# Kernel tuning notes

Hardware: AMD Instinct MI355X
Metric: run time of the kernel (lower is better)

## Reference

```python
import jax, jax.numpy as jnp
import numpy as np

B, A, F, C = 32, 64, 128, 128


def _mlp(h, W0, b0, W1, b1):
    # LinearLayer stack: Linear(2F->C) + ReLU, Linear(C->C) + ReLU
    h = jax.nn.relu(h @ W0 + b0)
    h = jax.nn.relu(h @ W1 + b1)
    return h


def setup_inputs() -> dict:
    key = jax.random.key(0)
    k0, k1, k2 = jax.random.split(key, 3)
    x = jax.random.normal(k0, (B, A, F), dtype=jnp.float32)
    W0 = jax.random.normal(k1, (2 * F, C), dtype=jnp.float32) * (1.0 / np.sqrt(2 * F))
    b0 = jnp.zeros((C,), dtype=jnp.float32)
    W1 = jax.random.normal(k2, (C, C), dtype=jnp.float32) * (1.0 / np.sqrt(C))
    b1 = jnp.zeros((C,), dtype=jnp.float32)
    return {"x": x, "W0": W0, "b0": b0, "W1": W1, "b1": b1}


def reference(x, W0, b0, W1, b1):
    nb, na, nf = x.shape
    # atom_tile[b,i,j]   = x[b,i]  (first atom of the pair)
    # atom_repeat[b,i,j] = x[b,j]  (second atom of the pair)
    xi = jnp.broadcast_to(x[:, :, None, :], (nb, na, na, nf))
    xj = jnp.broadcast_to(x[:, None, :, :], (nb, na, na, nf))
    # pair_x0 = cat(atom_tile, atom_repeat) = [x_i, x_j]
    p0 = jnp.concatenate([xi, xj], axis=-1).reshape(nb * na * na, 2 * nf)
    # pair_x1 = cat(atom_repeat, atom_tile) = [x_j, x_i]
    p1 = jnp.concatenate([xj, xi], axis=-1).reshape(nb * na * na, 2 * nf)
    h0 = _mlp(p0, W0, b0, W1, b1).reshape(nb, na * na, -1)
    h1 = _mlp(p1, W0, b0, W1, b1).reshape(nb, na * na, -1)
    return h0 + h1
```

## Files before the change

### kernel.cpp

```cpp
#include <hip/hip_runtime.h>
#include <hip/hip_bf16.h>

typedef float    f32x4 __attribute__((ext_vector_type(4)));
typedef _Float16 f16x8 __attribute__((ext_vector_type(8)));
typedef unsigned int   u32x4 __attribute__((ext_vector_type(4)));
typedef unsigned short u16x4 __attribute__((ext_vector_type(4)));

#define NB 32
#define NA 64
#define NF 128
#define NC 128

__global__ __launch_bounds__(512) void prep_kernel(
    const float* __restrict__ x, const float* __restrict__ W0,
    const float* __restrict__ b0, const float* __restrict__ W1,
    _Float16* __restrict__ u, _Float16* __restrict__ v,
    _Float16* __restrict__ w1f)
{
    int blk = blockIdx.x;
    int tid = threadIdx.x;
    if (blk < 256) {
        __shared__ __align__(16) float xs[8 * 128];
        int b = blk >> 3;
        int g = blk & 7;
        if (tid < 256)
            ((f32x4*)xs)[tid] =
                ((const f32x4*)(x + (size_t)(b * NA + g * 8) * NF))[tid];
        __syncthreads();
        int c = tid & 127;
        int h = (tid >> 7) & 1;
        int s = tid >> 8;
        const float* wp = W0 + (size_t)h * 128 * NC + c;
        const float* xp = xs + s * 4 * 128;
        float a0 = 0.f, a1 = 0.f, a2 = 0.f, a3 = 0.f;
        #pragma unroll 8
        for (int f = 0; f < 128; ++f) {
            float w = wp[(size_t)f * NC];
            a0 = fmaf(xp[f],       w, a0);
            a1 = fmaf(xp[128 + f], w, a1);
            a2 = fmaf(xp[256 + f], w, a2);
            a3 = fmaf(xp[384 + f], w, a3);
        }
        int row = b * NA + g * 8 + s * 4;
        if (h == 0) {
            u[(size_t)(row + 0) * NC + c] = (_Float16)a0;
            u[(size_t)(row + 1) * NC + c] = (_Float16)a1;
            u[(size_t)(row + 2) * NC + c] = (_Float16)a2;
            u[(size_t)(row + 3) * NC + c] = (_Float16)a3;
        } else {
            float bb = b0[c];
            v[(size_t)(row + 0) * NC + c] = (_Float16)(a0 + bb);
            v[(size_t)(row + 1) * NC + c] = (_Float16)(a1 + bb);
            v[(size_t)(row + 2) * NC + c] = (_Float16)(a2 + bb);
            v[(size_t)(row + 3) * NC + c] = (_Float16)(a3 + bb);
        }
    } else {
        int idx  = ((blk - 256) * 512 + tid) * 4;
        int e0   = idx & 7;
        int fl   = idx >> 3;
        int lane = fl & 63;
        int frag = fl >> 6;
        int kk = frag >> 3, nf = frag & 7;
        int k = kk * 32 + (lane >> 4) * 8 + e0;
        int n = nf * 16 + (lane & 15);
        u16x4 o;
        #pragma unroll
        for (int e = 0; e < 4; ++e) {
            _Float16 w = (_Float16)W1[(size_t)(k + e) * NC + n];
            o[e] = __builtin_bit_cast(unsigned short, w);
        }
        *(u16x4*)(w1f + idx) = o;
    }
}

__global__ __launch_bounds__(256, 3) void pair_mlp_kernel(
    const float* __restrict__ b1g, const _Float16* __restrict__ u,
    const _Float16* __restrict__ v, const _Float16* __restrict__ w1f,
    float* __restrict__ out)
{
    __shared__ __align__(16) _Float16 u_s[16 * 128];
    __shared__ __align__(16) _Float16 v_s[16 * 128];
    __shared__ __align__(16) _Float16 w_s[32 * 64 * 8];

    int blk = blockIdx.x;
    int b = blk / 36;
    int t = blk % 36;
    int I = 0;
    while (t >= 8 - I) { t -= 8 - I; ++I; }
    int J = I + t;

    int tid = threadIdx.x;

    {
        int row = tid >> 4;
        int c   = tid & 15;
        int ga  = b * NA + ((row < 8) ? (I * 8 + row) : (J * 8 + (row & 7)));
        ((u32x4*)u_s)[tid] = ((const u32x4*)(u + (size_t)ga * NC))[c];
        ((u32x4*)v_s)[tid] = ((const u32x4*)(v + (size_t)ga * NC))[c];
    }
    #pragma unroll
    for (int p = 0; p < 8; ++p)
        ((u32x4*)w_s)[p * 256 + tid] = ((const u32x4*)w1f)[p * 256 + tid];
    __syncthreads();

    int wave = tid >> 6;
    int lane = tid & 63;
    int llo  = lane & 15;
    int lhi  = lane >> 4;
    int r    = wave * 16 + llo;
    int il   = r >> 3;
    int jl   = r & 7;

    f32x4 acc0[8], acc1[8];
    f32x4 z = {0.f, 0.f, 0.f, 0.f};
    #pragma unroll
    for (int nf = 0; nf < 8; ++nf) { acc0[nf] = z; acc1[nf] = z; }

    const f16x8* uI = (const f16x8*)(u_s + il * 128);
    const f16x8* vI = (const f16x8*)(v_s + il * 128);
    const f16x8* uJ = (const f16x8*)(u_s + (8 + jl) * 128);
    const f16x8* vJ = (const f16x8*)(v_s + (8 + jl) * 128);
    const f16x8* wf = (const f16x8*)w_s;

    #pragma unroll
    for (int kk = 0; kk < 4; ++kk) {
        int kc = kk * 4 + lhi;

        f16x8 uIv = uI[kc];
        f16x8 vIv = vI[kc];
        f16x8 uJv = uJ[kc];
        f16x8 vJv = vJ[kc];

        f16x8 s0 = uIv + vJv;
        f16x8 s1 = uJv + vIv;
        f16x8 h0, h1;
        #pragma unroll
        for (int e = 0; e < 8; ++e) {
            h0[e] = s0[e] < (_Float16)0 ? (_Float16)0 : s0[e];
            h1[e] = s1[e] < (_Float16)0 ? (_Float16)0 : s1[e];
        }

        #pragma unroll
        for (int nf = 0; nf < 8; ++nf) {
            f16x8 w = wf[(kk * 8 + nf) * 64 + lane];
            acc0[nf] = __builtin_amdgcn_mfma_f32_16x16x32_f16(w, h0, acc0[nf], 0, 0, 0);
            acc1[nf] = __builtin_amdgcn_mfma_f32_16x16x32_f16(w, h1, acc1[nf], 0, 0, 0);
        }
    }

    int Ig = I * 8 + il;
    int Jg = J * 8 + jl;
    float* p1 = out + ((size_t)b * 4096 + Ig * 64 + Jg) * 128 + lhi * 4;
    float* p2 = out + ((size_t)b * 4096 + Jg * 64 + Ig) * 128 + lhi * 4;
    bool mirror = (I != J);
    #pragma unroll
    for (int nf = 0; nf < 8; ++nf) {
        f32x4 bias = *(const f32x4*)(b1g + nf * 16 + lhi * 4);
        f32x4 val;
        #pragma unroll
        for (int e = 0; e < 4; ++e)
            val[e] = fmaxf(acc0[nf][e] + bias[e], 0.f) +
                     fmaxf(acc1[nf][e] + bias[e], 0.f);
        *(f32x4*)(p1 + nf * 16) = val;
        if (mirror)
            *(f32x4*)(p2 + nf * 16) = val;
    }
}

extern "C" void kernel_launch(void* const* d_in, const int* in_sizes, int n_in,
                              void* d_out, int out_size, void* d_ws, size_t ws_size,
                              hipStream_t stream)
{
    (void)in_sizes; (void)n_in; (void)out_size; (void)ws_size;
    const float* x  = (const float*)d_in[0];
    const float* W0 = (const float*)d_in[1];
    const float* b0 = (const float*)d_in[2];
    const float* W1 = (const float*)d_in[3];
    const float* b1 = (const float*)d_in[4];
    float* out = (float*)d_out;

    _Float16* u   = (_Float16*)d_ws;
    _Float16* v   = u + (size_t)NB * NA * NC;
    _Float16* w1f = v + (size_t)NB * NA * NC;

    prep_kernel<<<264, 512, 0, stream>>>(x, W0, b0, W1, u, v, w1f);
    pair_mlp_kernel<<<32 * 36, 256, 0, stream>>>(b1, u, v, w1f, out);
}
```

Baseline: 32.33 us.

## Use MFMA for W0 projection in prep kernel and swizzle pair-kernel LDS

```diff
diff --git a/kernel.cpp b/kernel.cpp
--- a/kernel.cpp
+++ b/kernel.cpp
@@ -2,74 +2,104 @@
 #include <hip/hip_bf16.h>
 
 typedef float    f32x4 __attribute__((ext_vector_type(4)));
+typedef _Float16 f16x4 __attribute__((ext_vector_type(4)));
 typedef _Float16 f16x8 __attribute__((ext_vector_type(8)));
 typedef unsigned int   u32x4 __attribute__((ext_vector_type(4)));
-typedef unsigned short u16x4 __attribute__((ext_vector_type(4)));
 
 #define NB 32
 #define NA 64
 #define NF 128
 #define NC 128
 
-__global__ __launch_bounds__(512) void prep_kernel(
+__global__ __launch_bounds__(256) void prep_kernel(
     const float* __restrict__ x, const float* __restrict__ W0,
     const float* __restrict__ b0, const float* __restrict__ W1,
     _Float16* __restrict__ u, _Float16* __restrict__ v,
     _Float16* __restrict__ w1f)
 {
-    int blk = blockIdx.x;
-    int tid = threadIdx.x;
+    int blk = blockIdx.x, tid = threadIdx.x;
     if (blk < 256) {
-        __shared__ __align__(16) float xs[8 * 128];
-        int b = blk >> 3;
-        int g = blk & 7;
-        if (tid < 256)
-            ((f32x4*)xs)[tid] =
-                ((const f32x4*)(x + (size_t)(b * NA + g * 8) * NF))[tid];
+        __shared__ __align__(16) _Float16 w0h[32 * 64 * 8];
+        int b = blk >> 3, g = (blk >> 1) & 3, half = blk & 1;
+
+        int lane = tid & 63, wave = tid >> 6;
+        int llo = lane & 15, lhi = lane >> 4;
+
+        const float* xrow = x + ((size_t)b * NA + g * 16 + llo) * NF;
+        f16x8 xf[4];
+        #pragma unroll
+        for (int kk = 0; kk < 4; ++kk) {
+            f32x4 a0 = *(const f32x4*)(xrow + kk * 32 + lhi * 8);
+            f32x4 a1 = *(const f32x4*)(xrow + kk * 32 + lhi * 8 + 4);
+            #pragma unroll
+            for (int e = 0; e < 4; ++e) {
+                xf[kk][e]     = (_Float16)a0[e];
+                xf[kk][e + 4] = (_Float16)a1[e];
+            }
+        }
+
+        #pragma unroll
+        for (int p = 0; p < 8; ++p) {
+            int sl   = p * 256 + tid;
+            int frag = sl >> 6;
+            int ln   = sl & 63;
+            int kk   = frag >> 3, nfc = frag & 7;
+            int k0   = half * 128 + kk * 32 + (ln >> 4) * 8;
+            int c    = nfc * 16 + (ln & 15);
+            f16x8 o;
+            #pragma unroll
+            for (int e = 0; e < 8; ++e)
+                o[e] = (_Float16)W0[(size_t)(k0 + e) * NC + c];
+            *(f16x8*)(w0h + (size_t)sl * 8) = o;
+        }
         __syncthreads();
-        int c = tid & 127;
-        int h = (tid >> 7) & 1;
-        int s = tid >> 8;
-        const float* wp = W0 + (size_t)h * 128 * NC + c;
-        const float* xp = xs + s * 4 * 128;
-        float a0 = 0.f, a1 = 0.f, a2 = 0.f, a3 = 0.f;
-        #pragma unroll 8
-        for (int f = 0; f < 128; ++f) {
-            float w = wp[(size_t)f * NC];
-            a0 = fmaf(xp[f],       w, a0);
-            a1 = fmaf(xp[128 + f], w, a1);
-            a2 = fmaf(xp[256 + f], w, a2);
-            a3 = fmaf(xp[384 + f], w, a3);
-        }
-        int row = b * NA + g * 8 + s * 4;
-        if (h == 0) {
-            u[(size_t)(row + 0) * NC + c] = (_Float16)a0;
-            u[(size_t)(row + 1) * NC + c] = (_Float16)a1;
-            u[(size_t)(row + 2) * NC + c] = (_Float16)a2;
-            u[(size_t)(row + 3) * NC + c] = (_Float16)a3;
-        } else {
-            float bb = b0[c];
-            v[(size_t)(row + 0) * NC + c] = (_Float16)(a0 + bb);
-            v[(size_t)(row + 1) * NC + c] = (_Float16)(a1 + bb);
-            v[(size_t)(row + 2) * NC + c] = (_Float16)(a2 + bb);
-            v[(size_t)(row + 3) * NC + c] = (_Float16)(a3 + bb);
+
+        f32x4 acc[2];
+        f32x4 z = {0.f, 0.f, 0.f, 0.f};
+        acc[0] = z; acc[1] = z;
+        #pragma unroll
+        for (int kk = 0; kk < 4; ++kk) {
+            #pragma unroll
+            for (int t = 0; t < 2; ++t) {
+                int nfc = wave * 2 + t;
+                f16x8 aw = *(const f16x8*)(w0h +
+                    (size_t)((kk * 8 + nfc) * 64 + lane) * 8);
+                acc[t] = __builtin_amdgcn_mfma_f32_16x16x32_f16(
+                    aw, xf[kk], acc[t], 0, 0, 0);
+            }
+        }
+
+        _Float16* dst = half ? v : u;
+        size_t arow = ((size_t)b * NA + g * 16 + llo) * NC;
+        #pragma unroll
+        for (int t = 0; t < 2; ++t) {
+            int nfc = wave * 2 + t;
+            int c0  = nfc * 16 + lhi * 4;
+            f16x4 o;
+            if (half) {
+                f32x4 bb = *(const f32x4*)(b0 + c0);
+                #pragma unroll
+                for (int e = 0; e < 4; ++e)
+                    o[e] = (_Float16)(acc[t][e] + bb[e]);
+            } else {
+                #pragma unroll
+                for (int e = 0; e < 4; ++e)
+                    o[e] = (_Float16)acc[t][e];
+            }
+            *(f16x4*)(dst + arow + c0) = o;
         }
     } else {
-        int idx  = ((blk - 256) * 512 + tid) * 4;
-        int e0   = idx & 7;
-        int fl   = idx >> 3;
+        int fl   = (blk - 256) * 256 + tid;
         int lane = fl & 63;
         int frag = fl >> 6;
         int kk = frag >> 3, nf = frag & 7;
-        int k = kk * 32 + (lane >> 4) * 8 + e0;
-        int n = nf * 16 + (lane & 15);
-        u16x4 o;
-        #pragma unroll
-        for (int e = 0; e < 4; ++e) {
-            _Float16 w = (_Float16)W1[(size_t)(k + e) * NC + n];
-            o[e] = __builtin_bit_cast(unsigned short, w);
-        }
-        *(u16x4*)(w1f + idx) = o;
+        int k0 = kk * 32 + (lane >> 4) * 8;
+        int n  = nf * 16 + (lane & 15);
+        f16x8 o;
+        #pragma unroll
+        for (int e = 0; e < 8; ++e)
+            o[e] = (_Float16)W1[(size_t)(k0 + e) * NC + n];
+        *(f16x8*)(w1f + (size_t)fl * 8) = o;
     }
 }
 
@@ -95,8 +125,9 @@
         int row = tid >> 4;
         int c   = tid & 15;
         int ga  = b * NA + ((row < 8) ? (I * 8 + row) : (J * 8 + (row & 7)));
-        ((u32x4*)u_s)[tid] = ((const u32x4*)(u + (size_t)ga * NC))[c];
-        ((u32x4*)v_s)[tid] = ((const u32x4*)(v + (size_t)ga * NC))[c];
+        int sc  = row * 16 + (c ^ (row & 7));
+        ((u32x4*)u_s)[sc] = ((const u32x4*)(u + (size_t)ga * NC))[c];
+        ((u32x4*)v_s)[sc] = ((const u32x4*)(v + (size_t)ga * NC))[c];
     }
     #pragma unroll
     for (int p = 0; p < 8; ++p)
@@ -116,20 +147,20 @@
     #pragma unroll
     for (int nf = 0; nf < 8; ++nf) { acc0[nf] = z; acc1[nf] = z; }
 
-    const f16x8* uI = (const f16x8*)(u_s + il * 128);
-    const f16x8* vI = (const f16x8*)(v_s + il * 128);
-    const f16x8* uJ = (const f16x8*)(u_s + (8 + jl) * 128);
-    const f16x8* vJ = (const f16x8*)(v_s + (8 + jl) * 128);
+    const f16x8* us = (const f16x8*)u_s;
+    const f16x8* vs = (const f16x8*)v_s;
     const f16x8* wf = (const f16x8*)w_s;
 
     #pragma unroll
     for (int kk = 0; kk < 4; ++kk) {
-        int kc = kk * 4 + lhi;
-
-        f16x8 uIv = uI[kc];
-        f16x8 vIv = vI[kc];
-        f16x8 uJv = uJ[kc];
-        f16x8 vJv = vJ[kc];
+        int kc  = kk * 4 + lhi;
+        int scI = il * 16 + (kc ^ il);
+        int scJ = (8 + jl) * 16 + (kc ^ jl);
+
+        f16x8 uIv = us[scI];
+        f16x8 vIv = vs[scI];
+        f16x8 uJv = us[scJ];
+        f16x8 vJv = vs[scJ];
 
         f16x8 s0 = uIv + vJv;
         f16x8 s1 = uJv + vIv;
@@ -183,6 +214,6 @@
     _Float16* v   = u + (size_t)NB * NA * NC;
     _Float16* w1f = v + (size_t)NB * NA * NC;
 
-    prep_kernel<<<264, 512, 0, stream>>>(x, W0, b0, W1, u, v, w1f);
+    prep_kernel<<<264, 256, 0, stream>>>(x, W0, b0, W1, u, v, w1f);
     pair_mlp_kernel<<<32 * 36, 256, 0, stream>>>(b1, u, v, w1f, out);
 }
```

Measured after the change: 29.90 us. -7.5%, faster.
